# Performance work log

Hardware: AMD Instinct MI355X
Metric: run time of the kernel (lower is better)

## Reference

```python
import jax, jax.numpy as jnp
import numpy as np

V, D, H, L, F, S, B = 32000, 1024, 16, 6, 4096, 1024, 2
DK = D // H
SCALE = float(np.sqrt(DK))
NEG = -1e9


def _make_pe(max_len, d_model):
    pos = np.arange(max_len, dtype=np.float32)[:, None]
    div = np.exp(np.arange(0, d_model, 2, dtype=np.float32) * (-np.log(10000.0) / d_model))
    pe = np.zeros((max_len, d_model), dtype=np.float32)
    pe[:, 0::2] = np.sin(pos * div)
    pe[:, 1::2] = np.cos(pos * div)
    return jnp.asarray(pe)


def _ln(x, g, b, eps=1e-5):
    m = x.mean(-1, keepdims=True)
    v = ((x - m) ** 2).mean(-1, keepdims=True)
    return (x - m) / jnp.sqrt(v + eps) * g + b


def setup_inputs() -> dict:
    key = jax.random.key(0)
    ks = jax.random.split(key, 10)
    std = 0.02
    tokens = jax.random.randint(ks[0], (B, S), 0, V)
    emb = (jax.random.normal(ks[1], (V, D)) * std).at[0].set(0.0)  # padding_idx=0 row zeroed
    pe = _make_pe(4096, D)
    Wq = jax.random.normal(ks[2], (L, D, D)) * std
    Wk = jax.random.normal(ks[3], (L, D, D)) * std
    Wv = jax.random.normal(ks[4], (L, D, D)) * std
    Wo = jax.random.normal(ks[5], (L, D, D)) * std
    bo = jnp.zeros((L, D))
    g1 = jnp.ones((L, D)); be1 = jnp.zeros((L, D))
    g2 = jnp.ones((L, D)); be2 = jnp.zeros((L, D))
    W1 = jax.random.normal(ks[6], (L, D, F)) * std
    b1 = jnp.zeros((L, F))
    W2 = jax.random.normal(ks[7], (L, F, D)) * std
    b2 = jnp.zeros((L, D))
    gf = jnp.ones((D,)); bf = jnp.zeros((D,))
    Wout = jax.random.normal(ks[8], (D, V)) * std
    bout = jnp.zeros((V,))
    return dict(tokens=tokens, emb=emb, pe=pe, Wq=Wq, Wk=Wk, Wv=Wv, Wo=Wo, bo=bo,
                g1=g1, be1=be1, g2=g2, be2=be2, W1=W1, b1=b1, W2=W2, b2=b2,
                gf=gf, bf=bf, Wout=Wout, bout=bout)


def reference(tokens, emb, pe, Wq, Wk, Wv, Wo, bo, g1, be1, g2, be2,
              W1, b1, W2, b2, gf, bf, Wout, bout):
    Bx, Sx = tokens.shape
    x = emb[tokens] * jnp.sqrt(jnp.float32(D)) + pe[:Sx]  # (B,S,D)
    pad = tokens == 0  # (B,S) padding mask
    causal = jnp.triu(jnp.ones((Sx, Sx), dtype=bool), 1)
    mask = causal[None, None] | pad[:, None, None, :]  # (B,1,S,S), True = masked
    for l in range(L):
        h = _ln(x, g1[l], be1[l])
        q = (h @ Wq[l]).reshape(Bx, Sx, H, DK)
        k = (h @ Wk[l]).reshape(Bx, Sx, H, DK)
        v = (h @ Wv[l]).reshape(Bx, Sx, H, DK)
        scores = jnp.einsum('bqhd,bkhd->bhqk', q, k) / SCALE
        scores = jnp.where(mask, NEG, scores)  # masked_fill(mask, -1e9)
        a = jax.nn.softmax(scores, axis=-1)
        ctx = jnp.einsum('bhqk,bkhd->bqhd', a, v).reshape(Bx, Sx, D)
        x = x + ctx @ Wo[l] + bo[l]
        h = _ln(x, g2[l], be2[l])
        x = x + jax.nn.gelu(h @ W1[l] + b1[l], approximate=False) @ W2[l] + b2[l]
    x = _ln(x, gf, bf)
    return x @ Wout + bout  # (B,S,V)
```

## Files before the change

### kernel.cpp

```cpp
#include <hip/hip_runtime.h>
#include <hip/hip_bf16.h>
#include <stdint.h>

typedef __hip_bfloat16 bf16;
typedef __attribute__((ext_vector_type(8))) short bf16x8;
typedef __attribute__((ext_vector_type(4))) float f32x4;

#define DEV static __device__ __forceinline__

DEV float b2f(bf16 v) { return __bfloat162float(v); }
DEV bf16  f2b(float v) { return __float2bfloat16(v); }

DEV void gload16(const void* g, void* l) {
  __builtin_amdgcn_global_load_lds(
      (__attribute__((address_space(1))) void*)(void*)g,
      (__attribute__((address_space(3))) void*)l, 16, 0, 0);
}

DEV f32x4 mfma16(bf16x8 a, bf16x8 b, f32x4 c) {
  return __builtin_amdgcn_mfma_f32_16x16x32_bf16(a, b, c, 0, 0, 0);
}

__global__ __launch_bounds__(256) void embed_kernel(
    const int* __restrict__ tok, const float* __restrict__ emb,
    const float* __restrict__ pe, float* __restrict__ x)
{
  const int r = blockIdx.x, t = threadIdx.x;
  const int s = r & 1023;
  const int tk = tok[r];
  const int d = t * 4;
  const float* ep = emb + (size_t)tk * 1024 + d;
  const float* pp = pe + (size_t)s * 1024 + d;
  float* xp = x + (size_t)r * 1024 + d;
  #pragma unroll
  for (int j = 0; j < 4; ++j)
    xp[j] = ep[j] * 32.0f + pp[j];
}

__global__ __launch_bounds__(256) void ln_kernel(
    const float* __restrict__ x, const float* __restrict__ g,
    const float* __restrict__ be, bf16* __restrict__ h)
{
  const int r = blockIdx.x, t = threadIdx.x;
  const float4 v = ((const float4*)(x + (size_t)r * 1024))[t];
  float s  = v.x + v.y + v.z + v.w;
  float sq = v.x * v.x + v.y * v.y + v.z * v.z + v.w * v.w;
  #pragma unroll
  for (int d = 1; d < 64; d <<= 1) {
    s  += __shfl_xor(s, d);
    sq += __shfl_xor(sq, d);
  }
  __shared__ float red[8];
  const int w = t >> 6, l = t & 63;
  if (l == 0) { red[w] = s; red[4 + w] = sq; }
  __syncthreads();
  s  = red[0] + red[1] + red[2] + red[3];
  sq = red[4] + red[5] + red[6] + red[7];
  const float mean = s * (1.0f / 1024.0f);
  const float var  = sq * (1.0f / 1024.0f) - mean * mean;
  const float inv  = 1.0f / sqrtf(var + 1e-5f);
  bf16* hp = h + (size_t)r * 1024 + t * 4;
  const float* gp = g + t * 4;
  const float* bp = be + t * 4;
  const float vv[4] = {v.x, v.y, v.z, v.w};
  #pragma unroll
  for (int j = 0; j < 4; ++j)
    hp[j] = f2b((vv[j] - mean) * inv * gp[j] + bp[j]);
}

__global__ __launch_bounds__(256) void ln_res_kernel(
    float* __restrict__ x, const float* __restrict__ P, int np,
    const float* __restrict__ bias, const float* __restrict__ g,
    const float* __restrict__ be, bf16* __restrict__ h)
{
  const int r = blockIdx.x, t = threadIdx.x;
  float4 v = ((const float4*)(x + (size_t)r * 1024))[t];
  for (int i = 0; i < np; ++i) {
    const float4 pv = ((const float4*)(P + ((size_t)i * 2048 + r) * 1024))[t];
    v.x += pv.x; v.y += pv.y; v.z += pv.z; v.w += pv.w;
  }
  const float4 bv = ((const float4*)bias)[t];
  v.x += bv.x; v.y += bv.y; v.z += bv.z; v.w += bv.w;

  float s  = v.x + v.y + v.z + v.w;
  float sq = v.x * v.x + v.y * v.y + v.z * v.z + v.w * v.w;
  #pragma unroll
  for (int d = 1; d < 64; d <<= 1) {
    s  += __shfl_xor(s, d);
    sq += __shfl_xor(sq, d);
  }
  __shared__ float red[8];
  const int w = t >> 6, l = t & 63;
  if (l == 0) { red[w] = s; red[4 + w] = sq; }
  __syncthreads();
  s  = red[0] + red[1] + red[2] + red[3];
  sq = red[4] + red[5] + red[6] + red[7];
  const float mean = s * (1.0f / 1024.0f);
  const float var  = sq * (1.0f / 1024.0f) - mean * mean;
  const float inv  = 1.0f / sqrtf(var + 1e-5f);

  ((float4*)(x + (size_t)r * 1024))[t] = v;
  bf16* hp = h + (size_t)r * 1024 + t * 4;
  const float* gp = g + t * 4;
  const float* bp = be + t * 4;
  const float vv[4] = {v.x, v.y, v.z, v.w};
  #pragma unroll
  for (int j = 0; j < 4; ++j)
    hp[j] = f2b((vv[j] - mean) * inv * gp[j] + bp[j]);
}

DEV void transpose_tile(const float* __restrict__ in, bf16* __restrict__ out,
                        int ldin, int ldout, int r0, int c0, int t)
{
  __shared__ bf16 tile[64][64];
  #pragma unroll
  for (int i = 0; i < 4; ++i) {
    const int r = i * 16 + (t >> 4), c = (t & 15) * 4;
    const float4 v = *(const float4*)&in[(size_t)(r0 + r) * ldin + c0 + c];
    tile[r][c + 0] = f2b(v.x);
    tile[r][c + 1] = f2b(v.y);
    tile[r][c + 2] = f2b(v.z);
    tile[r][c + 3] = f2b(v.w);
  }
  __syncthreads();
  #pragma unroll
  for (int i = 0; i < 2; ++i) {
    const int oc = i * 32 + (t >> 3);
    const int rr = (t & 7) * 8;
    unsigned short tmp[8] __attribute__((aligned(16)));
    #pragma unroll
    for (int j = 0; j < 8; ++j)
      tmp[j] = ((const unsigned short*)tile)[(rr + j) * 64 + oc];
    *(uint4*)&out[(size_t)(c0 + oc) * ldout + r0 + rr] = *(const uint4*)tmp;
  }
}

__global__ __launch_bounds__(256) void transpose_cast_kernel(
    const float* __restrict__ in, bf16* __restrict__ out, int ldin, int ldout)
{
  transpose_tile(in, out, ldin, ldout, blockIdx.y * 64, blockIdx.x * 64, threadIdx.x);
}

DEV void prep_dispatch(int wid,
    const float* Wq, const float* Wk, const float* Wv, const float* Wo,
    const float* W1, const float* W2,
    bf16* WqkvT, bf16* WoT, bf16* W1T, bf16* W2T, int t)
{
  const float* src; bf16* dst; int ldin, ldout, tx, ty;
  if (wid < 768) {
    const int m = wid >> 8, tt = wid & 255;
    src = (m == 0) ? Wq : (m == 1) ? Wk : Wv;
    dst = WqkvT + (size_t)m * 1024 * 1024;
    ldin = 1024; ldout = 1024; tx = tt & 15; ty = tt >> 4;
  } else if (wid < 1024) {
    const int tt = wid - 768;
    src = Wo; dst = WoT; ldin = 1024; ldout = 1024; tx = tt & 15; ty = tt >> 4;
  } else if (wid < 2048) {
    const int tt = wid - 1024;
    src = W1; dst = W1T; ldin = 4096; ldout = 1024; tx = tt & 63; ty = tt >> 6;
  } else {
    const int tt = wid - 2048;
    src = W2; dst = W2T; ldin = 1024; ldout = 4096; tx = tt & 15; ty = tt >> 4;
  }
  transpose_tile(src, dst, ldin, ldout, ty * 64, tx * 64, t);
}

__global__ __launch_bounds__(256) void prep_layer_kernel(
    const float* __restrict__ Wq, const float* __restrict__ Wk,
    const float* __restrict__ Wv, const float* __restrict__ Wo,
    const float* __restrict__ W1, const float* __restrict__ W2,
    bf16* __restrict__ WqkvT, bf16* __restrict__ WoT,
    bf16* __restrict__ W1T, bf16* __restrict__ W2T)
{
  prep_dispatch(blockIdx.x, Wq, Wk, Wv, Wo, W1, W2,
                WqkvT, WoT, W1T, W2T, threadIdx.x);
}

__global__ __launch_bounds__(256) void prep_all_kernel(
    const float* __restrict__ Wq, const float* __restrict__ Wk,
    const float* __restrict__ Wv, const float* __restrict__ Wo,
    const float* __restrict__ W1, const float* __restrict__ W2,
    bf16* __restrict__ WqkvT, bf16* __restrict__ WoT,
    bf16* __restrict__ W1T, bf16* __restrict__ W2T)
{
  const int layer = blockIdx.x / 3072;
  const int wid = blockIdx.x - layer * 3072;
  const size_t DD = (size_t)1024 * 1024, DF = (size_t)1024 * 4096;
  prep_dispatch(wid,
      Wq + layer * DD, Wk + layer * DD, Wv + layer * DD, Wo + layer * DD,
      W1 + layer * DF, W2 + layer * DF,
      WqkvT + layer * 3 * DD, WoT + layer * DD,
      W1T + layer * DF, W2T + layer * DF, threadIdx.x);
}

__global__ __launch_bounds__(256) void transpose_v_kernel(
    const bf16* __restrict__ qkv, bf16* __restrict__ vT)
{
  __shared__ bf16 tile[64][64];
  const int t = threadIdx.x;
  const int s0 = blockIdx.x * 64;
  const int bh = blockIdx.y;
  const int b = bh >> 4, h = bh & 15;
  const bf16* in = qkv + (size_t)(b * 1024) * 3072 + 2048 + h * 64;
  #pragma unroll
  for (int i = 0; i < 2; ++i) {
    const int r = i * 32 + (t >> 3), c = (t & 7) * 8;
    *(uint4*)&tile[r][c] = *(const uint4*)&in[(size_t)(s0 + r) * 3072 + c];
  }
  __syncthreads();
  bf16* out = vT + (size_t)(bh * 64) * 1024;
  #pragma unroll
  for (int i = 0; i < 2; ++i) {
    const int oc = i * 32 + (t >> 3);
    const int rr = (t & 7) * 8;
    unsigned short tmp[8] __attribute__((aligned(16)));
    #pragma unroll
    for (int j = 0; j < 8; ++j)
      tmp[j] = ((const unsigned short*)tile)[(rr + j) * 64 + oc];
    *(uint4*)&out[(size_t)oc * 1024 + s0 + rr] = *(const uint4*)tmp;
  }
}

template<int EPI, int BM, int SWZ>
__global__ __launch_bounds__(256) void gemm_pl(
    const bf16* __restrict__ A, int lda,
    const bf16* __restrict__ BT, int ldb,
    void* __restrict__ Cp, int ldc,
    const float* __restrict__ bias,
    int ksl)
{
  constexpr int ABUF = BM * 32;
  constexpr int MR = BM / 32;
  __shared__ bf16 As[3 * ABUF];
  __shared__ bf16 Bs[3 * 4096];
  const int t = threadIdx.x;

  int bm, bn;
  if constexpr (SWZ) {
    const int nbm = gridDim.x;
    const int nwg = nbm * gridDim.y;
    int wid = blockIdx.x + nbm * blockIdx.y;
    wid = (wid & 7) * (nwg >> 3) + (wid >> 3);
    bm = wid % nbm; bn = wid / nbm;
  } else {
    bm = blockIdx.x; bn = blockIdx.y;
  }

  const int w = t >> 6, l = t & 63;
  const int wr = (w >> 1) * (BM / 2), wc = (w & 1) * 64;
  const int l15 = l & 15, l4 = l >> 4;
  const int kbeg = blockIdx.z * ksl;
  const int ntiles = ksl >> 5;

  const int colblk = (((t & 3) ^ ((t >> 3) & 3))) * 8;
  const bf16* gA = A  + (size_t)(bm * BM  + (t >> 2)) * lda + colblk + kbeg;
  const bf16* gB = BT + (size_t)(bn * 128 + (t >> 2)) * ldb + colblk + kbeg;
  bf16* lA = As + w * 512;
  bf16* lB = Bs + w * 512;

  auto stage = [&](int tile, int buf) {
    const int k0 = tile * 32;
    gload16(gA + k0, lA + buf * ABUF);
    if constexpr (BM == 128)
      gload16(gA + (size_t)64 * lda + k0, lA + buf * ABUF + 2048);
    gload16(gB + k0, lB + buf * 4096);
    gload16(gB + (size_t)64 * ldb + k0, lB + buf * 4096 + 2048);
  };

  f32x4 acc[MR][4];
  #pragma unroll
  for (int m = 0; m < MR; ++m)
    #pragma unroll
    for (int n = 0; n < 4; ++n)
      acc[m][n] = (f32x4){0.f, 0.f, 0.f, 0.f};

  stage(0, 0);
  stage(1, 1);

  const int rdcol = ((l4 ^ ((l15 >> 1) & 3))) * 8;

  int buf = 0;
  for (int kt = 0; kt < ntiles; ++kt) {
    if (kt + 2 < ntiles) {
      int pb = buf + 2; if (pb >= 3) pb -= 3;
      stage(kt + 2, pb);
      __builtin_amdgcn_sched_barrier(0);
      if constexpr (BM == 128) asm volatile("s_waitcnt vmcnt(8)" ::: "memory");
      else                     asm volatile("s_waitcnt vmcnt(6)" ::: "memory");
    } else if (kt + 1 < ntiles) {
      if constexpr (BM == 128) asm volatile("s_waitcnt vmcnt(4)" ::: "memory");
      else                     asm volatile("s_waitcnt vmcnt(3)" ::: "memory");
    } else {
      asm volatile("s_waitcnt vmcnt(0)" ::: "memory");
    }
    __builtin_amdgcn_s_barrier();
    __builtin_amdgcn_sched_barrier(0);

    const bf16* Ab = As + buf * ABUF;
    const bf16* Bb = Bs + buf * 4096;
    bf16x8 af[MR], bfr[4];
    #pragma unroll
    for (int m = 0; m < MR; ++m)
      af[m] = *(const bf16x8*)&Ab[(wr + m * 16 + l15) * 32 + rdcol];
    #pragma unroll
    for (int n = 0; n < 4; ++n)
      bfr[n] = *(const bf16x8*)&Bb[(wc + n * 16 + l15) * 32 + rdcol];
    #pragma unroll
    for (int m = 0; m < MR; ++m)
      #pragma unroll
      for (int n = 0; n < 4; ++n)
        acc[m][n] = mfma16(af[m], bfr[n], acc[m][n]);

    __builtin_amdgcn_sched_barrier(0);
    __builtin_amdgcn_s_barrier();
    if (++buf >= 3) buf = 0;
  }

  const int crow = bm * BM + wr, ccol = bn * 128 + wc;
  #pragma unroll
  for (int n = 0; n < 4; ++n) {
    const int col = ccol + n * 16 + l15;
    float bv = 0.f;
    if (EPI == 1 || EPI == 2) bv = bias[col];
    #pragma unroll
    for (int m = 0; m < MR; ++m) {
      const int row = crow + m * 16 + l4 * 4;
      #pragma unroll
      for (int r = 0; r < 4; ++r) {
        const float v = acc[m][n][r];
        if (EPI == 0) {
          ((bf16*)Cp)[(size_t)(row + r) * ldc + col] = f2b(v);
        } else if (EPI == 1) {
          ((float*)Cp)[(size_t)(row + r) * ldc + col] = v + bv;
        } else if (EPI == 2) {
          const float u = v + bv;
          const float gel = 0.5f * u * (1.0f + erff(u * 0.70710678118654752f));
          ((bf16*)Cp)[(size_t)(row + r) * ldc + col] = f2b(gel);
        } else {
          const int M = gridDim.x * BM;
          ((float*)Cp)[((size_t)blockIdx.z * M + row + r) * ldc + col] = v;
        }
      }
    }
  }
}

__global__ __launch_bounds__(512, 2) void gemm256(
    const bf16* __restrict__ A, int lda,
    const bf16* __restrict__ BT, int ldb,
    float* __restrict__ C, int ldc,
    const float* __restrict__ bias, int K)
{
  __shared__ bf16 As[3][8192];
  __shared__ bf16 Bs[3][8192];
  const int t = threadIdx.x;

  const int nbm = gridDim.x;
  const int nwg = nbm * gridDim.y;
  int wid = blockIdx.x + nbm * blockIdx.y;
  wid = (wid & 7) * (nwg >> 3) + (wid >> 3);
  const int bm = wid % nbm, bn = wid / nbm;

  const int w = t >> 6, l = t & 63;
  const int wm = w >> 2, wn = w & 3;
  const int l15 = l & 15, l4 = l >> 4;

  const int colblk = ((t & 3) ^ ((t >> 3) & 3)) * 8;
  const bf16* gA = A  + (size_t)(bm * 256 + (t >> 2)) * lda + colblk;
  const bf16* gB = BT + (size_t)(bn * 256 + (t >> 2)) * ldb + colblk;
  const int dst = w * 512;

  const int rd = (l4 ^ ((l15 >> 1) & 3)) * 8;
  const int arow = wm * 128 + l15;
  const int brow = wn * 64 + l15;

  f32x4 acc[8][4];
  #pragma unroll
  for (int m = 0; m < 8; ++m)
    #pragma unroll
    for (int n = 0; n < 4; ++n)
      acc[m][n] = (f32x4){0.f, 0.f, 0.f, 0.f};

  const int NT = K >> 5;

  auto stageA = [&](int kt, int buf) {
    const int k0 = kt * 32;
    gload16(gA + k0, &As[buf][dst]);
    gload16(gA + (size_t)128 * lda + k0, &As[buf][4096 + dst]);
  };
  auto stageB = [&](int kt, int buf) {
    const int k0 = kt * 32;
    gload16(gB + k0, &Bs[buf][dst]);
    gload16(gB + (size_t)128 * ldb + k0, &Bs[buf][4096 + dst]);
  };

  stageA(0, 0); stageB(0, 0);
  stageA(1, 1); stageB(1, 1);

  int buf = 0;
  for (int kt = 0; kt < NT; ++kt) {
    if (kt + 1 < NT) asm volatile("s_waitcnt vmcnt(4)" ::: "memory");
    else             asm volatile("s_waitcnt vmcnt(0)" ::: "memory");
    __builtin_amdgcn_s_barrier();
    __builtin_amdgcn_sched_barrier(0);

    int pb = buf + 2; if (pb >= 3) pb -= 3;
    const bf16* Ab = As[buf];
    const bf16* Bb = Bs[buf];

    bf16x8 bfr[4], af[4];
    #pragma unroll
    for (int n = 0; n < 4; ++n)
      bfr[n] = *(const bf16x8*)&Bb[(brow + n * 16) * 32 + rd];
    #pragma unroll
    for (int m = 0; m < 4; ++m)
      af[m] = *(const bf16x8*)&Ab[(arow + m * 16) * 32 + rd];
    if (kt + 2 < NT) stageA(kt + 2, pb);
    asm volatile("s_waitcnt lgkmcnt(0)" ::: "memory");
    __builtin_amdgcn_sched_barrier(0);
    __builtin_amdgcn_s_setprio(1);
    #pragma unroll
    for (int m = 0; m < 4; ++m)
      #pragma unroll
      for (int n = 0; n < 4; ++n)
        acc[m][n] = mfma16(af[m], bfr[n], acc[m][n]);
    __builtin_amdgcn_s_setprio(0);
    __builtin_amdgcn_sched_barrier(0);
    __builtin_amdgcn_s_barrier();

    #pragma unroll
    for (int m = 0; m < 4; ++m)
      af[m] = *(const bf16x8*)&Ab[(arow + (m + 4) * 16) * 32 + rd];
    if (kt + 2 < NT) stageB(kt + 2, pb);
    asm volatile("s_waitcnt lgkmcnt(0)" ::: "memory");
    __builtin_amdgcn_sched_barrier(0);
    __builtin_amdgcn_s_setprio(1);
    #pragma unroll
    for (int m = 0; m < 4; ++m)
      #pragma unroll
      for (int n = 0; n < 4; ++n)
        acc[m + 4][n] = mfma16(af[m], bfr[n], acc[m + 4][n]);
    __builtin_amdgcn_s_setprio(0);
    __builtin_amdgcn_sched_barrier(0);
    __builtin_amdgcn_s_barrier();

    if (++buf >= 3) buf = 0;
  }

  #pragma unroll
  for (int n = 0; n < 4; ++n) {
    const int col = bn * 256 + wn * 64 + n * 16 + l15;
    const float bv = bias[col];
    #pragma unroll
    for (int m = 0; m < 8; ++m) {
      const int row = bm * 256 + wm * 128 + m * 16 + l4 * 4;
      #pragma unroll
      for (int r = 0; r < 4; ++r)
        C[(size_t)(row + r) * ldc + col] = acc[m][n][r] + bv;
    }
  }
}

__global__ __launch_bounds__(256) void attn_kernel(
    const bf16* __restrict__ qkv, const bf16* __restrict__ vT,
    const int* __restrict__ tokens, bf16* __restrict__ ctx)
{
  __shared__ bf16 Ks[128 * 64];
  __shared__ bf16 VTs[64 * 128];
  __shared__ bf16 Ps[128 * 128];

  const int qt = blockIdx.x;
  const int bh = blockIdx.y;
  const int b = bh >> 4, h = bh & 15;
  const int t = threadIdx.x, w = t >> 6, l = t & 63;
  const int l15 = l & 15, l4 = l >> 4;
  const int q0 = qt * 128;

  bf16x8 aq[2][2];
  #pragma unroll
  for (int m = 0; m < 2; ++m)
    #pragma unroll
    for (int ks = 0; ks < 2; ++ks)
      aq[m][ks] = *(const bf16x8*)(qkv +
          (size_t)(b * 1024 + q0 + w * 32 + m * 16 + l15) * 3072 +
          h * 64 + ks * 32 + l4 * 8);

  f32x4 o[2][4];
  float m_run[2][4], l_run[2][4];
  #pragma unroll
  for (int m = 0; m < 2; ++m)
    #pragma unroll
    for (int r = 0; r < 4; ++r) { m_run[m][r] = -1e30f; l_run[m][r] = 0.f; }
  #pragma unroll
  for (int m = 0; m < 2; ++m)
    #pragma unroll
    for (int nn = 0; nn < 4; ++nn)
      o[m][nn] = (f32x4){0.f, 0.f, 0.f, 0.f};

  const bf16* kb = qkv + (size_t)(b * 1024) * 3072 + 1024 + h * 64;
  const bf16* vb = vT + (size_t)(bh * 64) * 1024;
  const int* tb = tokens + b * 1024;

  const int kSrcCol = ((t & 7) ^ ((t >> 3) & 7)) * 8;
  const int vSrcCol = ((t & 15) ^ (t >> 4)) * 8;

  for (int jt = 0; jt <= qt; ++jt) {
    const int j0 = jt * 128;
    __syncthreads();
    #pragma unroll
    for (int i = 0; i < 4; ++i)
      gload16(kb + (size_t)(j0 + i * 32 + (t >> 3)) * 3072 + kSrcCol,
              Ks + i * 2048 + w * 512);
    #pragma unroll
    for (int i = 0; i < 4; ++i)
      gload16(vb + (size_t)(i * 16 + (t >> 4)) * 1024 + j0 + vSrcCol,
              VTs + i * 2048 + w * 512);
    __syncthreads();

    f32x4 s[2][8];
    #pragma unroll
    for (int m = 0; m < 2; ++m)
      #pragma unroll
      for (int n = 0; n < 8; ++n)
        s[m][n] = (f32x4){0.f, 0.f, 0.f, 0.f};
    #pragma unroll
    for (int ks = 0; ks < 2; ++ks) {
      #pragma unroll
      for (int n = 0; n < 8; ++n) {
        const bf16x8 bk = *(const bf16x8*)
            &Ks[(n * 16 + l15) * 64 + ((ks * 32 + l4 * 8) ^ ((l15 & 7) * 8))];
        #pragma unroll
        for (int m = 0; m < 2; ++m)
          s[m][n] = mfma16(aq[m][ks], bk, s[m][n]);
      }
    }

    float padv[8];
    #pragma unroll
    for (int n = 0; n < 8; ++n)
      padv[n] = (tb[j0 + n * 16 + l15] == 0) ? 1.f : 0.f;

    #pragma unroll
    for (int m = 0; m < 2; ++m) {
      #pragma unroll
      for (int r = 0; r < 4; ++r) {
        const int rloc = l4 * 4 + r;
        const int qrow = q0 + w * 32 + m * 16 + rloc;
        float vals[8];
        float mx = -1e30f;
        #pragma unroll
        for (int n = 0; n < 8; ++n) {
          const int jg = j0 + n * 16 + l15;
          float v = s[m][n][r] * 0.125f;
          if (jg > qrow || padv[n] != 0.f) v = -1e9f;
          vals[n] = v;
          mx = fmaxf(mx, v);
        }
        #pragma unroll
        for (int d = 1; d < 16; d <<= 1) mx = fmaxf(mx, __shfl_xor(mx, d));
        const float newm = fmaxf(m_run[m][r], mx);
        const float sc = __expf(m_run[m][r] - newm);
        m_run[m][r] = newm;
        float rs = 0.f;
        #pragma unroll
        for (int n = 0; n < 8; ++n) {
          const float pv = __expf(vals[n] - newm);
          vals[n] = pv;
          rs += pv;
        }
        #pragma unroll
        for (int d = 1; d < 16; d <<= 1) rs += __shfl_xor(rs, d);
        l_run[m][r] = l_run[m][r] * sc + rs;
        #pragma unroll
        for (int nn = 0; nn < 4; ++nn) o[m][nn][r] = o[m][nn][r] * sc;
        #pragma unroll
        for (int n = 0; n < 8; ++n)
          Ps[(w * 32 + m * 16 + rloc) * 128 +
             ((n * 16 + l15) ^ (rloc * 8))] = f2b(vals[n]);
      }
    }
    __syncthreads();

    #pragma unroll
    for (int ks = 0; ks < 4; ++ks) {
      bf16x8 ap[2];
      #pragma unroll
      for (int m = 0; m < 2; ++m)
        ap[m] = *(const bf16x8*)
            &Ps[(w * 32 + m * 16 + l15) * 128 + ((ks * 32 + l4 * 8) ^ (l15 * 8))];
      #pragma unroll
      for (int nn = 0; nn < 4; ++nn) {
        const bf16x8 bv = *(const bf16x8*)
            &VTs[(nn * 16 + l15) * 128 + ((ks * 32 + l4 * 8) ^ (l15 * 8))];
        #pragma unroll
        for (int m = 0; m < 2; ++m)
          o[m][nn] = mfma16(ap[m], bv, o[m][nn]);
      }
    }
  }

  #pragma unroll
  for (int m = 0; m < 2; ++m) {
    #pragma unroll
    for (int r = 0; r < 4; ++r) {
      const float inv = 1.0f / l_run[m][r];
      const int qrow = q0 + w * 32 + m * 16 + l4 * 4 + r;
      #pragma unroll
      for (int nn = 0; nn < 4; ++nn)
        ctx[(size_t)(b * 1024 + qrow) * 1024 + h * 64 + nn * 16 + l15] =
            f2b(o[m][nn][r] * inv);
    }
  }
}

__global__ __launch_bounds__(64) void attn_fixup_kernel(
    const int* __restrict__ tokens, const bf16* __restrict__ vT,
    bf16* __restrict__ ctx)
{
  const int bh = blockIdx.x;
  const int b = bh >> 4, h = bh & 15;
  __shared__ int p0s;
  if (threadIdx.x == 0) {
    int p = 0;
    const int* tb = tokens + b * 1024;
    while (p < 1024 && tb[p] == 0) ++p;
    p0s = p;
  }
  __syncthreads();
  const int P0 = p0s;
  if (P0 == 0) return;
  const int dk = threadIdx.x;
  const bf16* vrow = vT + (size_t)(bh * 64 + dk) * 1024;
  float sum = 0.f;
  for (int sIdx = 0; sIdx < 1024; ++sIdx) sum += b2f(vrow[sIdx]);
  const bf16 mv = f2b(sum * (1.0f / 1024.0f));
  for (int q = 0; q < P0; ++q)
    ctx[(size_t)(b * 1024 + q) * 1024 + h * 64 + dk] = mv;
}

extern "C" void kernel_launch(void* const* d_in, const int* in_sizes, int n_in,
                              void* d_out, int out_size, void* d_ws, size_t ws_size,
                              hipStream_t stream)
{
  (void)in_sizes; (void)n_in; (void)out_size;
  const int*   tokens = (const int*)d_in[0];
  const float* emb  = (const float*)d_in[1];
  const float* pe   = (const float*)d_in[2];
  const float* Wq   = (const float*)d_in[3];
  const float* Wk   = (const float*)d_in[4];
  const float* Wv   = (const float*)d_in[5];
  const float* Wo   = (const float*)d_in[6];
  const float* bo   = (const float*)d_in[7];
  const float* g1   = (const float*)d_in[8];
  const float* be1  = (const float*)d_in[9];
  const float* g2   = (const float*)d_in[10];
  const float* be2  = (const float*)d_in[11];
  const float* W1   = (const float*)d_in[12];
  const float* b1   = (const float*)d_in[13];
  const float* W2   = (const float*)d_in[14];
  const float* b2   = (const float*)d_in[15];
  const float* gf   = (const float*)d_in[16];
  const float* bff  = (const float*)d_in[17];
  const float* Wout = (const float*)d_in[18];
  const float* bout = (const float*)d_in[19];
  float* out = (float*)d_out;

  char* p = (char*)d_ws;
  auto alloc = [&](size_t bytes) {
    char* q = p;
    p += (bytes + 255) & ~(size_t)255;
    return q;
  };
  float* x    = (float*)alloc((size_t)2048 * 1024 * 4);
  float* Pp   = (float*)alloc((size_t)4 * 2048 * 1024 * 4);
  bf16* h     = (bf16*)alloc((size_t)2048 * 1024 * 2);
  bf16* qkv   = (bf16*)alloc((size_t)2048 * 3072 * 2);
  bf16* vT    = (bf16*)alloc((size_t)2048 * 1024 * 2);
  bf16* ctx   = (bf16*)alloc((size_t)2048 * 1024 * 2);
  bf16* ff    = (bf16*)alloc((size_t)2048 * 4096 * 2);
  bf16* WoutT = (bf16*)alloc((size_t)32000 * 1024 * 2);

  const size_t DD = (size_t)1024 * 1024;
  const size_t DF = (size_t)1024 * 4096;

  const size_t perLayerW = (3 * DD + DD + DF + DF) * 2;
  const size_t used = (size_t)(p - (char*)d_ws);
  const bool fullprep = ws_size >= used + 6 * perLayerW + 8192;
  const int NL = fullprep ? 6 : 1;
  bf16* WqkvT = (bf16*)alloc((size_t)NL * 3 * DD * 2);
  bf16* WoT   = (bf16*)alloc((size_t)NL * DD * 2);
  bf16* W1T   = (bf16*)alloc((size_t)NL * DF * 2);
  bf16* W2T   = (bf16*)alloc((size_t)NL * DF * 2);

  if (fullprep)
    prep_all_kernel<<<6 * 3072, 256, 0, stream>>>(
        Wq, Wk, Wv, Wo, W1, W2, WqkvT, WoT, W1T, W2T);

  embed_kernel<<<2048, 256, 0, stream>>>(tokens, emb, pe, x);

  for (int l = 0; l < 6; ++l) {
    const bf16* wqkvt; const bf16* wot; const bf16* w1t; const bf16* w2t;
    if (fullprep) {
      wqkvt = WqkvT + (size_t)l * 3 * DD;
      wot   = WoT   + (size_t)l * DD;
      w1t   = W1T   + (size_t)l * DF;
      w2t   = W2T   + (size_t)l * DF;
    } else {
      prep_layer_kernel<<<3072, 256, 0, stream>>>(
          Wq + l * DD, Wk + l * DD, Wv + l * DD, Wo + l * DD,
          W1 + l * DF, W2 + l * DF, WqkvT, WoT, W1T, W2T);
      wqkvt = WqkvT; wot = WoT; w1t = W1T; w2t = W2T;
    }

    if (l == 0)
      ln_kernel<<<2048, 256, 0, stream>>>(x, g1, be1, h);
    else
      ln_res_kernel<<<2048, 256, 0, stream>>>(
          x, Pp, 4, b2 + (l - 1) * 1024, g1 + l * 1024, be1 + l * 1024, h);

    gemm_pl<0, 64, 0><<<dim3(32, 24, 1), 256, 0, stream>>>(
        h, 1024, wqkvt, 1024, qkv, 3072, (const float*)nullptr, 1024);
    transpose_v_kernel<<<dim3(16, 32), 256, 0, stream>>>(qkv, vT);
    attn_kernel<<<dim3(8, 32), 256, 0, stream>>>(qkv, vT, tokens, ctx);
    attn_fixup_kernel<<<32, 64, 0, stream>>>(tokens, vT, ctx);
    gemm_pl<3, 64, 0><<<dim3(32, 8, 2), 256, 0, stream>>>(
        ctx, 1024, wot, 1024, Pp, 1024, (const float*)nullptr, 512);
    ln_res_kernel<<<2048, 256, 0, stream>>>(
        x, Pp, 2, bo + l * 1024, g2 + l * 1024, be2 + l * 1024, h);
    gemm_pl<2, 128, 0><<<dim3(16, 32, 1), 256, 0, stream>>>(
        h, 1024, w1t, 1024, ff, 4096, b1 + l * 4096, 1024);
    gemm_pl<3, 128, 0><<<dim3(16, 8, 4), 256, 0, stream>>>(
        ff, 4096, w2t, 4096, Pp, 1024, (const float*)nullptr, 1024);
  }

  ln_res_kernel<<<2048, 256, 0, stream>>>(x, Pp, 4, b2 + 5 * 1024, gf, bff, h);
  transpose_cast_kernel<<<dim3(500, 16), 256, 0, stream>>>(Wout, WoutT, 32000, 1024);
  gemm256<<<dim3(8, 125), 512, 0, stream>>>(
      h, 1024, WoutT, 1024, out, 32000, bout, 1024);
}
```

Measured before the change: 1.475 ms.

## Store split-K partials in bf16, widen attention blocks, retile QKV and Wo GEMMs

Split-K GEMM partial sums are now written and read as bf16 instead of fp32, halving partial-buffer traffic into the residual LayerNorm kernels. The attention kernel moves to 512 threads with one 16-row tile per wave, and the barrier before the P·V step is replaced by a local LDS waitcnt. The QKV GEMM switches to 128-row tiles, and the Wo GEMM uses 128-row tiles with 4-way split-K. Rounding partial sums to bf16 before accumulating them reduces accuracy of the residual stream.

```diff
diff --git a/kernel.cpp b/kernel.cpp
--- a/kernel.cpp
+++ b/kernel.cpp
@@ -10,6 +10,13 @@
 
 DEV float b2f(bf16 v) { return __bfloat162float(v); }
 DEV bf16  f2b(float v) { return __float2bfloat16(v); }
+
+DEV float u2f(unsigned short u) {
+  unsigned int x = (unsigned int)u << 16;
+  float f;
+  __builtin_memcpy(&f, &x, 4);
+  return f;
+}
 
 DEV void gload16(const void* g, void* l) {
   __builtin_amdgcn_global_load_lds(
@@ -69,15 +76,15 @@
 }
 
 __global__ __launch_bounds__(256) void ln_res_kernel(
-    float* __restrict__ x, const float* __restrict__ P, int np,
+    float* __restrict__ x, const bf16* __restrict__ P, int np,
     const float* __restrict__ bias, const float* __restrict__ g,
     const float* __restrict__ be, bf16* __restrict__ h)
 {
   const int r = blockIdx.x, t = threadIdx.x;
   float4 v = ((const float4*)(x + (size_t)r * 1024))[t];
   for (int i = 0; i < np; ++i) {
-    const float4 pv = ((const float4*)(P + ((size_t)i * 2048 + r) * 1024))[t];
-    v.x += pv.x; v.y += pv.y; v.z += pv.z; v.w += pv.w;
+    const ushort4 pv = ((const ushort4*)(P + ((size_t)i * 2048 + r) * 1024))[t];
+    v.x += u2f(pv.x); v.y += u2f(pv.y); v.z += u2f(pv.z); v.w += u2f(pv.w);
   }
   const float4 bv = ((const float4*)bias)[t];
   v.x += bv.x; v.y += bv.y; v.z += bv.z; v.w += bv.w;
@@ -338,7 +345,7 @@
           ((bf16*)Cp)[(size_t)(row + r) * ldc + col] = f2b(gel);
         } else {
           const int M = gridDim.x * BM;
-          ((float*)Cp)[((size_t)blockIdx.z * M + row + r) * ldc + col] = v;
+          ((bf16*)Cp)[((size_t)blockIdx.z * M + row + r) * ldc + col] = f2b(v);
         }
       }
     }
@@ -461,7 +468,7 @@
   }
 }
 
-__global__ __launch_bounds__(256) void attn_kernel(
+__global__ __launch_bounds__(512) void attn_kernel(
     const bf16* __restrict__ qkv, const bf16* __restrict__ vT,
     const int* __restrict__ tokens, bf16* __restrict__ ctx)
 {
@@ -476,62 +483,52 @@
   const int l15 = l & 15, l4 = l >> 4;
   const int q0 = qt * 128;
 
-  bf16x8 aq[2][2];
-  #pragma unroll
-  for (int m = 0; m < 2; ++m)
-    #pragma unroll
-    for (int ks = 0; ks < 2; ++ks)
-      aq[m][ks] = *(const bf16x8*)(qkv +
-          (size_t)(b * 1024 + q0 + w * 32 + m * 16 + l15) * 3072 +
-          h * 64 + ks * 32 + l4 * 8);
-
-  f32x4 o[2][4];
-  float m_run[2][4], l_run[2][4];
-  #pragma unroll
-  for (int m = 0; m < 2; ++m)
-    #pragma unroll
-    for (int r = 0; r < 4; ++r) { m_run[m][r] = -1e30f; l_run[m][r] = 0.f; }
-  #pragma unroll
-  for (int m = 0; m < 2; ++m)
-    #pragma unroll
-    for (int nn = 0; nn < 4; ++nn)
-      o[m][nn] = (f32x4){0.f, 0.f, 0.f, 0.f};
+  bf16x8 aq[2];
+  #pragma unroll
+  for (int ks = 0; ks < 2; ++ks)
+    aq[ks] = *(const bf16x8*)(qkv +
+        (size_t)(b * 1024 + q0 + w * 16 + l15) * 3072 +
+        h * 64 + ks * 32 + l4 * 8);
+
+  f32x4 o[4];
+  float m_run[4], l_run[4];
+  #pragma unroll
+  for (int r = 0; r < 4; ++r) { m_run[r] = -1e30f; l_run[r] = 0.f; }
+  #pragma unroll
+  for (int nn = 0; nn < 4; ++nn)
+    o[nn] = (f32x4){0.f, 0.f, 0.f, 0.f};
 
   const bf16* kb = qkv + (size_t)(b * 1024) * 3072 + 1024 + h * 64;
   const bf16* vb = vT + (size_t)(bh * 64) * 1024;
   const int* tb = tokens + b * 1024;
 
   const int kSrcCol = ((t & 7) ^ ((t >> 3) & 7)) * 8;
-  const int vSrcCol = ((t & 15) ^ (t >> 4)) * 8;
+  const int vSrcCol = ((t & 15) ^ ((t >> 4) & 15)) * 8;
 
   for (int jt = 0; jt <= qt; ++jt) {
     const int j0 = jt * 128;
     __syncthreads();
     #pragma unroll
-    for (int i = 0; i < 4; ++i)
-      gload16(kb + (size_t)(j0 + i * 32 + (t >> 3)) * 3072 + kSrcCol,
-              Ks + i * 2048 + w * 512);
-    #pragma unroll
-    for (int i = 0; i < 4; ++i)
-      gload16(vb + (size_t)(i * 16 + (t >> 4)) * 1024 + j0 + vSrcCol,
-              VTs + i * 2048 + w * 512);
+    for (int i = 0; i < 2; ++i)
+      gload16(kb + (size_t)(j0 + i * 64 + (t >> 3)) * 3072 + kSrcCol,
+              Ks + i * 4096 + w * 512);
+    #pragma unroll
+    for (int i = 0; i < 2; ++i)
+      gload16(vb + (size_t)(i * 32 + (t >> 4)) * 1024 + j0 + vSrcCol,
+              VTs + i * 4096 + w * 512);
     __syncthreads();
 
-    f32x4 s[2][8];
-    #pragma unroll
-    for (int m = 0; m < 2; ++m)
-      #pragma unroll
-      for (int n = 0; n < 8; ++n)
-        s[m][n] = (f32x4){0.f, 0.f, 0.f, 0.f};
+    f32x4 s[8];
+    #pragma unroll
+    for (int n = 0; n < 8; ++n)
+      s[n] = (f32x4){0.f, 0.f, 0.f, 0.f};
     #pragma unroll
     for (int ks = 0; ks < 2; ++ks) {
       #pragma unroll
       for (int n = 0; n < 8; ++n) {
         const bf16x8 bk = *(const bf16x8*)
             &Ks[(n * 16 + l15) * 64 + ((ks * 32 + l4 * 8) ^ ((l15 & 7) * 8))];
-        #pragma unroll
-        for (int m = 0; m < 2; ++m)
-          s[m][n] = mfma16(aq[m][ks], bk, s[m][n]);
+        s[n] = mfma16(aq[ks], bk, s[n]);
       }
     }
 
@@ -541,75 +538,63 @@
       padv[n] = (tb[j0 + n * 16 + l15] == 0) ? 1.f : 0.f;
 
     #pragma unroll
-    for (int m = 0; m < 2; ++m) {
-      #pragma unroll
-      for (int r = 0; r < 4; ++r) {
-        const int rloc = l4 * 4 + r;
-        const int qrow = q0 + w * 32 + m * 16 + rloc;
-        float vals[8];
-        float mx = -1e30f;
-        #pragma unroll
-        for (int n = 0; n < 8; ++n) {
-          const int jg = j0 + n * 16 + l15;
-          float v = s[m][n][r] * 0.125f;
-          if (jg > qrow || padv[n] != 0.f) v = -1e9f;
-          vals[n] = v;
-          mx = fmaxf(mx, v);
-        }
-        #pragma unroll
-        for (int d = 1; d < 16; d <<= 1) mx = fmaxf(mx, __shfl_xor(mx, d));
-        const float newm = fmaxf(m_run[m][r], mx);
-        const float sc = __expf(m_run[m][r] - newm);
-        m_run[m][r] = newm;
-        float rs = 0.f;
-        #pragma unroll
-        for (int n = 0; n < 8; ++n) {
-          const float pv = __expf(vals[n] - newm);
-          vals[n] = pv;
-          rs += pv;
-        }
-        #pragma unroll
-        for (int d = 1; d < 16; d <<= 1) rs += __shfl_xor(rs, d);
-        l_run[m][r] = l_run[m][r] * sc + rs;
-        #pragma unroll
-        for (int nn = 0; nn < 4; ++nn) o[m][nn][r] = o[m][nn][r] * sc;
-        #pragma unroll
-        for (int n = 0; n < 8; ++n)
-          Ps[(w * 32 + m * 16 + rloc) * 128 +
-             ((n * 16 + l15) ^ (rloc * 8))] = f2b(vals[n]);
+    for (int r = 0; r < 4; ++r) {
+      const int rloc = l4 * 4 + r;
+      const int qrow = q0 + w * 16 + rloc;
+      float vals[8];
+      float mx = -1e30f;
+      #pragma unroll
+      for (int n = 0; n < 8; ++n) {
+        const int jg = j0 + n * 16 + l15;
+        float v = s[n][r] * 0.125f;
+        if (jg > qrow || padv[n] != 0.f) v = -1e9f;
+        vals[n] = v;
+        mx = fmaxf(mx, v);
       }
+      #pragma unroll
+      for (int d = 1; d < 16; d <<= 1) mx = fmaxf(mx, __shfl_xor(mx, d));
+      const float newm = fmaxf(m_run[r], mx);
+      const float sc = __expf(m_run[r] - newm);
+      m_run[r] = newm;
+      float rs = 0.f;
+      #pragma unroll
+      for (int n = 0; n < 8; ++n) {
+        const float pv = __expf(vals[n] - newm);
+        vals[n] = pv;
+        rs += pv;
+      }
+      #pragma unroll
+      for (int d = 1; d < 16; d <<= 1) rs += __shfl_xor(rs, d);
+      l_run[r] = l_run[r] * sc + rs;
+      #pragma unroll
+      for (int nn = 0; nn < 4; ++nn) o[nn][r] = o[nn][r] * sc;
+      #pragma unroll
+      for (int n = 0; n < 8; ++n)
+        Ps[(w * 16 + rloc) * 128 + ((n * 16 + l15) ^ (rloc * 8))] = f2b(vals[n]);
     }
-    __syncthreads();
+    asm volatile("s_waitcnt lgkmcnt(0)" ::: "memory");
 
     #pragma unroll
     for (int ks = 0; ks < 4; ++ks) {
-      bf16x8 ap[2];
-      #pragma unroll
-      for (int m = 0; m < 2; ++m)
-        ap[m] = *(const bf16x8*)
-            &Ps[(w * 32 + m * 16 + l15) * 128 + ((ks * 32 + l4 * 8) ^ (l15 * 8))];
+      const bf16x8 ap = *(const bf16x8*)
+          &Ps[(w * 16 + l15) * 128 + ((ks * 32 + l4 * 8) ^ (l15 * 8))];
       #pragma unroll
       for (int nn = 0; nn < 4; ++nn) {
         const bf16x8 bv = *(const bf16x8*)
             &VTs[(nn * 16 + l15) * 128 + ((ks * 32 + l4 * 8) ^ (l15 * 8))];
-        #pragma unroll
-        for (int m = 0; m < 2; ++m)
-          o[m][nn] = mfma16(ap[m], bv, o[m][nn]);
+        o[nn] = mfma16(ap, bv, o[nn]);
       }
     }
   }
 
   #pragma unroll
-  for (int m = 0; m < 2; ++m) {
-    #pragma unroll
-    for (int r = 0; r < 4; ++r) {
-      const float inv = 1.0f / l_run[m][r];
-      const int qrow = q0 + w * 32 + m * 16 + l4 * 4 + r;
-      #pragma unroll
-      for (int nn = 0; nn < 4; ++nn)
-        ctx[(size_t)(b * 1024 + qrow) * 1024 + h * 64 + nn * 16 + l15] =
-            f2b(o[m][nn][r] * inv);
-    }
+  for (int r = 0; r < 4; ++r) {
+    const float inv = 1.0f / l_run[r];
+    const int qrow = q0 + w * 16 + l4 * 4 + r;
+    #pragma unroll
+    for (int nn = 0; nn < 4; ++nn)
+      ctx[(size_t)(b * 1024 + qrow) * 1024 + h * 64 + nn * 16 + l15] =
+          f2b(o[nn][r] * inv);
   }
 }
 
@@ -672,7 +657,7 @@
     return q;
   };
   float* x    = (float*)alloc((size_t)2048 * 1024 * 4);
-  float* Pp   = (float*)alloc((size_t)4 * 2048 * 1024 * 4);
+  bf16* Pp    = (bf16*)alloc((size_t)4 * 2048 * 1024 * 2);
   bf16* h     = (bf16*)alloc((size_t)2048 * 1024 * 2);
   bf16* qkv   = (bf16*)alloc((size_t)2048 * 3072 * 2);
   bf16* vT    = (bf16*)alloc((size_t)2048 * 1024 * 2);
@@ -718,15 +703,15 @@
       ln_res_kernel<<<2048, 256, 0, stream>>>(
           x, Pp, 4, b2 + (l - 1) * 1024, g1 + l * 1024, be1 + l * 1024, h);
 
-    gemm_pl<0, 64, 0><<<dim3(32, 24, 1), 256, 0, stream>>>(
+    gemm_pl<0, 128, 0><<<dim3(16, 24, 1), 256, 0, stream>>>(
         h, 1024, wqkvt, 1024, qkv, 3072, (const float*)nullptr, 1024);
     transpose_v_kernel<<<dim3(16, 32), 256, 0, stream>>>(qkv, vT);
-    attn_kernel<<<dim3(8, 32), 256, 0, stream>>>(qkv, vT, tokens, ctx);
+    attn_kernel<<<dim3(8, 32), 512, 0, stream>>>(qkv, vT, tokens, ctx);
     attn_fixup_kernel<<<32, 64, 0, stream>>>(tokens, vT, ctx);
-    gemm_pl<3, 64, 0><<<dim3(32, 8, 2), 256, 0, stream>>>(
-        ctx, 1024, wot, 1024, Pp, 1024, (const float*)nullptr, 512);
+    gemm_pl<3, 128, 0><<<dim3(16, 8, 4), 256, 0, stream>>>(
+        ctx, 1024, wot, 1024, Pp, 1024, (const float*)nullptr, 256);
     ln_res_kernel<<<2048, 256, 0, stream>>>(
-        x, Pp, 2, bo + l * 1024, g2 + l * 1024, be2 + l * 1024, h);
+        x, Pp, 4, bo + l * 1024, g2 + l * 1024, be2 + l * 1024, h);
     gemm_pl<2, 128, 0><<<dim3(16, 32, 1), 256, 0, stream>>>(
         h, 1024, w1t, 1024, ff, 4096, b1 + l * 4096, 1024);
     gemm_pl<3, 128, 0><<<dim3(16, 8, 4), 256, 0, stream>>>(
```

Result: faster. 1.347 ms (-8.6%).
